# Kernel tuning notes

Measured on AMD Instinct MI355X. Metric: run time of the kernel, lower is better.

Reference implementation:

```python
import jax, jax.numpy as jnp
import numpy as np


def conv1d(x, w, b, pad):
    # x: [B, C, L], w: [O, C, K], torch nn.Conv1d semantics (cross-correlation + bias)
    y = jax.lax.conv_general_dilated(
        x, w, window_strides=(1,), padding=[(pad, pad)],
        dimension_numbers=("NCH", "OIH", "NCH"))
    return y + b[None, :, None]


def setup_inputs() -> dict:
    key = jax.random.key(0)
    ks = jax.random.split(key, 11)
    B, C, L = 32, 4, 65536
    def rn(k, shape, fan_in):
        # kaiming-ish scale so activations stay sane
        return jax.random.normal(k, shape, dtype=jnp.float32) / np.sqrt(fan_in)
    return {
        "x": jax.random.normal(ks[0], (B, C, L), dtype=jnp.float32),
        "w_motif": rn(ks[1], (40, 4, 51), 4 * 51),
        "b_motif": jnp.zeros((40,), jnp.float32),
        "w_reduce": rn(ks[2], (4, 40, 1), 40),
        "b_reduce": jnp.zeros((4,), jnp.float32),
        "w_fft": rn(ks[3], (4, 4, 401), 4 * 401),
        "b_fft": jnp.zeros((4,), jnp.float32),
        "w_expand": rn(ks[4], (40, 4, 1), 4),
        "b_expand": jnp.zeros((40,), jnp.float32),
        "w_effect": rn(ks[5], (2, 40, 601), 40 * 601),
        "b_effect": jnp.zeros((2,), jnp.float32),
    }


def reference(x, w_motif, b_motif, w_reduce, b_reduce, w_fft, b_fft,
              w_expand, b_expand, w_effect, b_effect):
    # motif layer + softplus
    y = jax.nn.softplus(conv1d(x, w_motif, b_motif, 25))          # [B,40,L]
    # synergy: factorized FFT-conv block (reduce 1x1 -> long conv -> expand 1x1)
    s = conv1d(y, w_reduce, b_reduce, 0)                          # [B,4,L]
    s = conv1d(s, w_fft, b_fft, 200)                              # [B,4,L]
    s = conv1d(s, w_expand, b_expand, 0)                          # [B,40,L]
    motifact = jax.nn.sigmoid(s) * y                              # gated
    # effect: long conv -> sigmoid
    y_pred = jax.nn.sigmoid(conv1d(motifact, w_effect, b_effect, 300))  # [B,2,L]
    return y_pred[:, :, 500:-500]
```

## Files before the change

kernel.cpp:

```cpp
#include <hip/hip_runtime.h>
#include <hip/hip_bf16.h>
#include <math.h>

#define LEN 65536
#define LOUT 64536
typedef __hip_bfloat16 bf16;
typedef __attribute__((ext_vector_type(8))) short short8;
typedef __attribute__((ext_vector_type(4))) float f32x4;

__device__ inline float b2f(bf16 h) { return __bfloat162float(h); }
__device__ inline bf16 f2b(float f) { return __float2bfloat16(f); }
__device__ inline float us2f(unsigned short u) { bf16 h = *(bf16*)&u; return __bfloat162float(h); }
__device__ inline float softplus_f(float v) {
    return fmaxf(v, 0.f) + __logf(1.f + __expf(-fabsf(v)));
}

__global__ __launch_bounds__(256) void k_x2b(const float* __restrict__ x,
                                             short* __restrict__ xb, int n8) {
    int i = blockIdx.x * 256 + threadIdx.x;
    if (i >= n8) return;
    const float* src = x + (size_t)i * 8;
    float4 f0 = *(const float4*)src;
    float4 f1 = *(const float4*)(src + 4);
    short8 v; bf16 h;
    h = f2b(f0.x); v[0] = *(short*)&h;
    h = f2b(f0.y); v[1] = *(short*)&h;
    h = f2b(f0.z); v[2] = *(short*)&h;
    h = f2b(f0.w); v[3] = *(short*)&h;
    h = f2b(f1.x); v[4] = *(short*)&h;
    h = f2b(f1.y); v[5] = *(short*)&h;
    h = f2b(f1.z); v[6] = *(short*)&h;
    h = f2b(f1.w); v[7] = *(short*)&h;
    *(short8*)(xb + (size_t)i * 8) = v;
}

__global__ __launch_bounds__(256) void k_prep_mot(const float* __restrict__ w_motif,
                                                  short* __restrict__ fragA) {
    int idx = blockIdx.x * 256 + threadIdx.x;
    if (idx >= 40 * 4 * 3 * 64 * 8) return;
    int i = idx & 7;
    int lane = (idx >> 3) & 63;
    int rest = idx >> 9;
    int qc = rest % 3; rest /= 3;
    int c = rest & 3; int o = rest >> 2;
    int dlt = lane & 15, kb = lane >> 4;
    int m = 32 * qc + 8 * kb + i;
    int k = m - 7 - dlt;
    float v = (k >= 0 && k < 51) ? w_motif[(o * 4 + c) * 51 + k] : 0.f;
    bf16 h = f2b(v);
    fragA[idx] = *(short*)&h;
}

#define MOT_BLKS 522
#define MOT_PAD  528
__global__ __launch_bounds__(256, 2) void k_motif_mfma(const short* __restrict__ xb,
        const short* __restrict__ fragA, const float* __restrict__ b_motif,
        bf16* __restrict__ y, int b0) {
    __shared__ __align__(16) short bwin[4][MOT_PAD * 8];
    const int tid = threadIdx.x;
    const int lane = tid & 63, wv = tid >> 6;
    const int wg = blockIdx.x, bl = blockIdx.y, og = blockIdx.z;
    const int bg = b0 + bl;
    const int L0 = wg * 4096;
    const int win0 = L0 - 32;
    const int ln15 = lane & 15, lkb = lane >> 4;

    short8 af[4][12];
    #pragma unroll
    for (int Mt = 0; Mt < 4; ++Mt)
        #pragma unroll
        for (int kq = 0; kq < 12; ++kq)
            af[Mt][kq] = *(const short8*)(fragA +
                (size_t)(((og * 4 + Mt) * 12 + kq) * 64 + lane) * 8);

    #pragma unroll 1
    for (int c = 0; c < 4; ++c) {
        const short* src = xb + ((size_t)bg * 4 + c) * LEN;
        for (int Lb = tid; Lb < MOT_BLKS; Lb += 256) {
            int gi = win0 + Lb * 8;
            short8 v;
            if (gi >= 0 && gi + 8 <= LEN) {
                v = *(const short8*)(src + gi);
            } else {
                #pragma unroll
                for (int j = 0; j < 8; ++j)
                    v[j] = (gi + j >= 0 && gi + j < LEN) ? src[gi + j] : (short)0;
            }
            int Pb = Lb ^ ((Lb >> 3) & 7);
            *(short8*)(&bwin[c][Pb * 8]) = v;
        }
    }
    __syncthreads();

    #pragma unroll 1
    for (int nt = 0; nt < 4; ++nt) {
        const int tt = wv * 4 + nt;
        f32x4 acc[4];
        #pragma unroll
        for (int Mt = 0; Mt < 4; ++Mt) acc[Mt] = (f32x4){0.f, 0.f, 0.f, 0.f};
        #pragma unroll
        for (int c = 0; c < 4; ++c) {
            #pragma unroll
            for (int qc = 0; qc < 3; ++qc) {
                int L = 32 * tt + 2 * ln15 + 4 * qc + lkb;
                int P = L ^ ((L >> 3) & 7);
                short8 bfr = *(const short8*)(&bwin[c][P * 8]);
                #pragma unroll
                for (int Mt = 0; Mt < 4; ++Mt)
                    acc[Mt] = __builtin_amdgcn_mfma_f32_16x16x32_bf16(
                        af[Mt][c * 3 + qc], bfr, acc[Mt], 0, 0, 0);
            }
        }
        #pragma unroll
        for (int Mt = 0; Mt < 4; ++Mt) {
            float bb = b_motif[og * 4 + Mt];
            int pos = L0 + tt * 256 + 16 * ln15 + 4 * lkb;
            ushort4 st; bf16 h;
            float v0 = softplus_f(acc[Mt][0] + bb);
            float v1 = softplus_f(acc[Mt][1] + bb);
            float v2 = softplus_f(acc[Mt][2] + bb);
            float v3 = softplus_f(acc[Mt][3] + bb);
            h = f2b(v0); st.x = *(unsigned short*)&h;
            h = f2b(v1); st.y = *(unsigned short*)&h;
            h = f2b(v2); st.z = *(unsigned short*)&h;
            h = f2b(v3); st.w = *(unsigned short*)&h;
            *(ushort4*)(&y[((size_t)bl * 40 + og * 4 + Mt) * LEN + pos]) = st;
        }
    }
}

__global__ __launch_bounds__(256) void k_reduce(const short* __restrict__ y,
        const float* __restrict__ w_reduce, const float* __restrict__ b_reduce,
        bf16* __restrict__ s1) {
    const int tid = threadIdx.x;
    const int bl = blockIdx.y;
    const int l8 = (blockIdx.x * 256 + tid) * 8;
    float s[4][8];
    #pragma unroll
    for (int c = 0; c < 4; ++c)
        #pragma unroll
        for (int e = 0; e < 8; ++e) s[c][e] = b_reduce[c];
    #pragma unroll 1
    for (int o = 0; o < 40; ++o) {
        short8 v = *(const short8*)(y + ((size_t)bl * 40 + o) * LEN + l8);
        float yv[8];
        #pragma unroll
        for (int e = 0; e < 8; ++e) yv[e] = us2f((unsigned short)v[e]);
        #pragma unroll
        for (int c = 0; c < 4; ++c) {
            float w = w_reduce[c * 40 + o];
            #pragma unroll
            for (int e = 0; e < 8; ++e) s[c][e] += w * yv[e];
        }
    }
    #pragma unroll
    for (int c = 0; c < 4; ++c) {
        short8 st; bf16 h;
        #pragma unroll
        for (int e = 0; e < 8; ++e) { h = f2b(s[c][e]); st[e] = *(short*)&h; }
        *(short8*)(&s1[((size_t)bl * 4 + c) * LEN + l8]) = st;
    }
}

__global__ __launch_bounds__(256) void k_prep_fft(const float* __restrict__ w_fft,
                                                  short* __restrict__ fragA) {
    int idx = blockIdx.x * 256 + threadIdx.x;
    if (idx >= 4 * 7 * 4 * 2 * 64 * 8) return;
    int i = idx & 7;
    int lane = (idx >> 3) & 63;
    int rest = idx >> 9;
    int ql = rest & 1; rest >>= 1;
    int Mt = rest & 3; rest >>= 2;
    int qb = rest % 7; int c = rest / 7;
    int dlt = lane & 15, kb = lane >> 4;
    int kkp = 32 * (qb * 2 + ql) + 8 * kb + i;
    int kk = kkp - dlt;
    float v = (kk >= 0 && kk < 401) ? w_fft[(Mt * 4 + c) * 401 + kk] : 0.f;
    bf16 h = f2b(v);
    fragA[idx] = *(short*)&h;
}

#define FFT_BLKS 568
__global__ __launch_bounds__(256) void k_fft(const short* __restrict__ s1,
        const short* __restrict__ fragA, const float* __restrict__ b_fft,
        bf16* __restrict__ s2) {
    __shared__ __align__(16) short bwin[4][FFT_BLKS * 8];
    const int tid = threadIdx.x;
    const int lane = tid & 63, wv = tid >> 6;
    const int wg = blockIdx.x, bl = blockIdx.y;
    const int P0 = wg * 4096;
    const int win0 = P0 - 200;
    const int ln15 = lane & 15, lkb = lane >> 4;

    f32x4 acc[4][4];
    #pragma unroll
    for (int Mt = 0; Mt < 4; ++Mt)
        #pragma unroll
        for (int nt = 0; nt < 4; ++nt)
            acc[Mt][nt] = (f32x4){0.f, 0.f, 0.f, 0.f};

    #pragma unroll 1
    for (int cl = 0; cl < 4; ++cl) {
        const short* src = s1 + ((size_t)bl * 4 + cl) * LEN;
        for (int Lb = tid; Lb < FFT_BLKS; Lb += 256) {
            int gi = win0 + Lb * 8;
            short8 v;
            if (gi >= 0 && gi + 8 <= LEN) {
                v = *(const short8*)(src + gi);
            } else {
                #pragma unroll
                for (int j = 0; j < 8; ++j)
                    v[j] = (gi + j >= 0 && gi + j < LEN) ? src[gi + j] : (short)0;
            }
            int Pb = Lb ^ ((Lb >> 3) & 7);
            *(short8*)(&bwin[cl][Pb * 8]) = v;
        }
    }
    __syncthreads();

    #pragma unroll 1
    for (int cl = 0; cl < 4; ++cl) {
        #pragma unroll 1
        for (int qb = 0; qb < 7; ++qb) {
            short8 af[4][2];
            #pragma unroll
            for (int Mt = 0; Mt < 4; ++Mt)
                #pragma unroll
                for (int ql = 0; ql < 2; ++ql)
                    af[Mt][ql] = *(const short8*)(fragA +
                        (size_t)((((cl * 7 + qb) * 4 + Mt) * 2 + ql) * 64 + lane) * 8);
            #pragma unroll
            for (int nt = 0; nt < 4; ++nt) {
                const int tt = wv * 4 + nt;
                #pragma unroll
                for (int ql = 0; ql < 2; ++ql) {
                    int qc = qb * 2 + ql;
                    int L = 2 * ln15 + lkb + 4 * qc + 32 * tt;
                    int P = L ^ ((L >> 3) & 7);
                    short8 bfr = *(const short8*)(&bwin[cl][P * 8]);
                    #pragma unroll
                    for (int Mt = 0; Mt < 4; ++Mt)
                        acc[Mt][nt] = __builtin_amdgcn_mfma_f32_16x16x32_bf16(
                            af[Mt][ql], bfr, acc[Mt][nt], 0, 0, 0);
                }
            }
        }
    }

    #pragma unroll
    for (int Mt = 0; Mt < 4; ++Mt) {
        float bb = b_fft[Mt];
        #pragma unroll
        for (int nt = 0; nt < 4; ++nt) {
            int tt = wv * 4 + nt;
            int pos = P0 + tt * 256 + 16 * ln15 + 4 * lkb;
            ushort4 st; bf16 h;
            h = f2b(acc[Mt][nt][0] + bb); st.x = *(unsigned short*)&h;
            h = f2b(acc[Mt][nt][1] + bb); st.y = *(unsigned short*)&h;
            h = f2b(acc[Mt][nt][2] + bb); st.z = *(unsigned short*)&h;
            h = f2b(acc[Mt][nt][3] + bb); st.w = *(unsigned short*)&h;
            *(ushort4*)(&s2[((size_t)bl * 4 + Mt) * LEN + pos]) = st;
        }
    }
}

__global__ __launch_bounds__(256) void k_prep(const float* __restrict__ w_eff,
                                              short* __restrict__ fragA) {
    int idx = blockIdx.x * 256 + threadIdx.x;
    if (idx >= 40 * 4 * 2 * 5 * 64 * 8) return;
    int i = idx & 7;
    int lane = (idx >> 3) & 63;
    int rest = idx >> 9;
    int ql = rest % 5; rest /= 5;
    int Mt = rest & 1; rest >>= 1;
    int qb = rest & 3; int c = rest >> 2;
    int q = qb * 5 + ql;
    int dlt = lane & 15, kb = lane >> 4;
    int kp = 32 * q + 8 * kb + i;
    int kk = kp - dlt;
    float v = (kk >= 0 && kk < 601) ? w_eff[(Mt * 40 + c) * 601 + kk] : 0.f;
    bf16 h = __float2bfloat16(v);
    fragA[idx] = *(short*)&h;
}

#define EFF_NBLK 336
#define EFF_SH (EFF_NBLK * 8)
__device__ __forceinline__ void eff_prefetch(const short* __restrict__ mact,
        size_t chanBase, int cc, int tid, int win0, short8 (&yreg)[2][4]) {
    #pragma unroll
    for (int it = 0; it < 2; ++it) {
        int Lb = tid + it * 256;
        if (Lb < EFF_NBLK) {
            int gi = win0 + Lb * 8;
            bool full = (gi + 8 <= LEN);
            #pragma unroll
            for (int ch = 0; ch < 4; ++ch) {
                const short* src = mact + (chanBase + cc * 4 + ch) * (size_t)LEN;
                short8 v = {0, 0, 0, 0, 0, 0, 0, 0};
                if (full) {
                    v = *(const short8*)(src + gi);
                } else {
                    #pragma unroll
                    for (int j = 0; j < 8; ++j)
                        v[j] = (gi + j < LEN) ? src[gi + j] : (short)0;
                }
                yreg[it][ch] = v;
            }
        }
    }
}

__global__ __launch_bounds__(256, 3) void k_effect(const short* __restrict__ mact,
        const short* __restrict__ s2,
        const short* __restrict__ fragA,
        const float* __restrict__ w_expand, const float* __restrict__ b_expand,
        float* __restrict__ part) {
    __shared__ __align__(16) char smem[2 * EFF_SH * 4 * 2 + 160 * 4 + 40 * 4];
    short (*bwin)[EFF_SH]  = (short(*)[EFF_SH])smem;
    short (*s2win)[EFF_SH] = (short(*)[EFF_SH])(smem + EFF_SH * 4 * 2);
    float* wexp = (float*)(smem + 2 * EFF_SH * 4 * 2);
    float* bexp = wexp + 160;
    float* red  = (float*)smem;

    const int tid = threadIdx.x;
    const int lane = tid & 63, wv = tid >> 6;
    const int wgl = blockIdx.x, bl = blockIdx.y, half = blockIdx.z;
    const int coff = half * 20;
    const int L0 = wgl * 2048;
    const int win0 = L0 + 200;
    const int ln15 = lane & 15, lkb = lane >> 4;
    const size_t chanBase = (size_t)bl * 40 + coff;

    if (tid < 160) wexp[tid] = w_expand[tid];
    if (tid < 40) bexp[tid] = b_expand[tid];
    #pragma unroll 1
    for (int c = 0; c < 4; ++c) {
        const short* sp = s2 + ((size_t)bl * 4 + c) * LEN;
        for (int Lb = tid; Lb < EFF_NBLK; Lb += 256) {
            int gi = win0 + Lb * 8;
            short8 v = {0, 0, 0, 0, 0, 0, 0, 0};
            if (gi + 8 <= LEN) {
                v = *(const short8*)(sp + gi);
            } else {
                #pragma unroll
                for (int j = 0; j < 8; ++j)
                    v[j] = (gi + j < LEN) ? sp[gi + j] : (short)0;
            }
            *(short8*)(&s2win[c][Lb * 8]) = v;
        }
    }

    f32x4 acc[2][8];
    #pragma unroll
    for (int Mt = 0; Mt < 2; ++Mt)
        #pragma unroll
        for (int tt = 0; tt < 8; ++tt)
            acc[Mt][tt] = (f32x4){0.f, 0.f, 0.f, 0.f};

    short8 yreg[2][4];
    eff_prefetch(mact, chanBase, 0, tid, win0, yreg);

    #pragma unroll 1
    for (int cc = 0; cc < 5; ++cc) {
        __syncthreads();
        #pragma unroll
        for (int it = 0; it < 2; ++it) {
            int Lb = tid + it * 256;
            if (Lb < EFF_NBLK) {
                float s2v[4][8];
                #pragma unroll
                for (int c = 0; c < 4; ++c) {
                    short8 sv = *(const short8*)(&s2win[c][Lb * 8]);
                    #pragma unroll
                    for (int j = 0; j < 8; ++j) s2v[c][j] = us2f((unsigned short)sv[j]);
                }
                int P = Lb ^ ((Lb >> 3) & 7);
                #pragma unroll
                for (int ch = 0; ch < 4; ++ch) {
                    int o = coff + cc * 4 + ch;
                    float w0 = wexp[o * 4 + 0], w1 = wexp[o * 4 + 1];
                    float w2 = wexp[o * 4 + 2], w3 = wexp[o * 4 + 3];
                    float be = bexp[o];
                    short8 w;
                    #pragma unroll
                    for (int j = 0; j < 8; ++j) {
                        float sg = be + w0 * s2v[0][j] + w1 * s2v[1][j]
                                      + w2 * s2v[2][j] + w3 * s2v[3][j];
                        float g = __builtin_amdgcn_rcpf(1.f + __expf(-sg));
                        float yv = us2f((unsigned short)yreg[it][ch][j]) * g;
                        bf16 h = f2b(yv);
                        w[j] = *(short*)&h;
                    }
                    *(short8*)(&bwin[ch][P * 8]) = w;
                }
            }
        }
        __syncthreads();
        if (cc < 4) eff_prefetch(mact, chanBase, cc + 1, tid, win0, yreg);
        const int cg = coff + cc * 4 + wv;
        #pragma unroll 1
        for (int qb = 0; qb < 4; ++qb) {
            short8 af[2][5];
            #pragma unroll
            for (int Mt = 0; Mt < 2; ++Mt)
                #pragma unroll
                for (int ql = 0; ql < 5; ++ql)
                    af[Mt][ql] = *(const short8*)(fragA +
                        (size_t)(((((cg * 4 + qb) * 2 + Mt) * 5 + ql) * 64 + lane) * 8));
            #pragma unroll
            for (int tt = 0; tt < 8; ++tt) {
                #pragma unroll
                for (int ql = 0; ql < 5; ++ql) {
                    int q = qb * 5 + ql;
                    int L = 32 * tt + 2 * ln15 + 4 * q + lkb;
                    int P = L ^ ((L >> 3) & 7);
                    short8 bfr = *(const short8*)(&bwin[wv][P * 8]);
                    acc[0][tt] = __builtin_amdgcn_mfma_f32_16x16x32_bf16(
                        af[0][ql], bfr, acc[0][tt], 0, 0, 0);
                    acc[1][tt] = __builtin_amdgcn_mfma_f32_16x16x32_bf16(
                        af[1][ql], bfr, acc[1][tt], 0, 0, 0);
                }
            }
        }
    }

    __syncthreads();
    if (wv == 1 || wv == 3) {
        float* p = red + (wv >> 1) * 4096;
        #pragma unroll
        for (int Mt = 0; Mt < 2; ++Mt)
            #pragma unroll
            for (int tt = 0; tt < 8; ++tt)
                *(f32x4*)(p + (Mt * 8 + tt) * 256 + lane * 4) = acc[Mt][tt];
    }
    __syncthreads();
    if (wv == 0 || wv == 2) {
        float* p = red + (wv >> 1) * 4096;
        #pragma unroll
        for (int Mt = 0; Mt < 2; ++Mt)
            #pragma unroll
            for (int tt = 0; tt < 8; ++tt)
                acc[Mt][tt] += *(const f32x4*)(p + (Mt * 8 + tt) * 256 + lane * 4);
    }
    __syncthreads();
    if (wv == 2) {
        #pragma unroll
        for (int Mt = 0; Mt < 2; ++Mt)
            #pragma unroll
            for (int tt = 0; tt < 8; ++tt)
                *(f32x4*)(red + (Mt * 8 + tt) * 256 + lane * 4) = acc[Mt][tt];
    }
    __syncthreads();
    if (wv == 0) {
        #pragma unroll
        for (int Mt = 0; Mt < 2; ++Mt) {
            #pragma unroll
            for (int tt = 0; tt < 8; ++tt) {
                f32x4 a = acc[Mt][tt];
                a += *(const f32x4*)(red + (Mt * 8 + tt) * 256 + lane * 4);
                int pos = L0 + tt * 256 + 16 * ln15 + 4 * lkb;
                float4 st; st.x = a[0]; st.y = a[1]; st.z = a[2]; st.w = a[3];
                *(float4*)(&part[(((size_t)bl * 2 + half) * 2 + Mt) * LEN + pos]) = st;
            }
        }
    }
}

__global__ __launch_bounds__(256) void k_comb(const float* __restrict__ part,
        const float* __restrict__ b_eff, float* __restrict__ out, int b0) {
    const int tid = threadIdx.x;
    const int bl = blockIdx.y, bg = b0 + bl;
    int l4 = (blockIdx.x * 256 + tid) * 4;
    if (l4 >= LOUT) return;
    #pragma unroll
    for (int Mt = 0; Mt < 2; ++Mt) {
        float bb = b_eff[Mt];
        float4 p0 = *(const float4*)(&part[(((size_t)bl * 2 + 0) * 2 + Mt) * LEN + l4]);
        float4 p1 = *(const float4*)(&part[(((size_t)bl * 2 + 1) * 2 + Mt) * LEN + l4]);
        float4 st;
        st.x = __builtin_amdgcn_rcpf(1.f + __expf(-(p0.x + p1.x + bb)));
        st.y = __builtin_amdgcn_rcpf(1.f + __expf(-(p0.y + p1.y + bb)));
        st.z = __builtin_amdgcn_rcpf(1.f + __expf(-(p0.z + p1.z + bb)));
        st.w = __builtin_amdgcn_rcpf(1.f + __expf(-(p0.w + p1.w + bb)));
        *(float4*)(&out[((size_t)bg * 2 + Mt) * LOUT + l4]) = st;
    }
}

extern "C" void kernel_launch(void* const* d_in, const int* in_sizes, int n_in,
                              void* d_out, int out_size, void* d_ws, size_t ws_size,
                              hipStream_t stream) {
    const float* x        = (const float*)d_in[0];
    const float* w_motif  = (const float*)d_in[1];
    const float* b_motif  = (const float*)d_in[2];
    const float* w_reduce = (const float*)d_in[3];
    const float* b_reduce = (const float*)d_in[4];
    const float* w_fft    = (const float*)d_in[5];
    const float* b_fft    = (const float*)d_in[6];
    const float* w_expand = (const float*)d_in[7];
    const float* b_expand = (const float*)d_in[8];
    const float* w_eff    = (const float*)d_in[9];
    const float* b_eff    = (const float*)d_in[10];
    float* out = (float*)d_out;

    const size_t FRAGA_EFF = (size_t)40 * 4 * 2 * 5 * 64 * 8 * 2;
    const size_t FRAGA_FFT = (size_t)4 * 7 * 4 * 2 * 64 * 8 * 2;
    const size_t FRAGA_MOT = (size_t)40 * 4 * 3 * 64 * 8 * 2;
    const size_t XB_B      = (size_t)32 * 4 * LEN * 2;
    const size_t HEAD = FRAGA_EFF + FRAGA_FFT + FRAGA_MOT + XB_B;

    short* fragA_eff = (short*)d_ws;
    short* fragA_fft = (short*)((char*)d_ws + FRAGA_EFF);
    short* fragA_mot = (short*)((char*)d_ws + FRAGA_EFF + FRAGA_FFT);
    short* xb        = (short*)((char*)d_ws + FRAGA_EFF + FRAGA_FFT + FRAGA_MOT);
    char*  rest      = (char*)d_ws + HEAD;

    const size_t PB_Y = (size_t)40 * LEN * 2;
    const size_t PB_S = (size_t)4 * LEN * 2;
    const size_t PERB = PB_Y + 2 * PB_S + (size_t)2 * 2 * LEN * 4;
    size_t avail = (ws_size > HEAD) ? (ws_size - HEAD) : 0;
    int nb = (int)(avail / PERB);
    if (nb > 32) nb = 32;
    if (nb < 1) nb = 1;

    bf16*  y    = (bf16*)rest;
    bf16*  s1   = (bf16*)(rest + PB_Y * (size_t)nb);
    bf16*  s2   = (bf16*)(rest + (PB_Y + PB_S) * (size_t)nb);
    float* part = (float*)(rest + (PB_Y + 2 * PB_S) * (size_t)nb);

    hipLaunchKernelGGL(k_prep,     dim3(3200), dim3(256), 0, stream, w_eff, fragA_eff);
    hipLaunchKernelGGL(k_prep_fft, dim3(448),  dim3(256), 0, stream, w_fft, fragA_fft);
    hipLaunchKernelGGL(k_prep_mot, dim3(960),  dim3(256), 0, stream, w_motif, fragA_mot);
    hipLaunchKernelGGL(k_x2b,      dim3(4096), dim3(256), 0, stream, x, xb,
                       (int)(32 * 4 * LEN / 8));

    for (int b0 = 0; b0 < 32; b0 += nb) {
        int nbb = (32 - b0 < nb) ? (32 - b0) : nb;
        hipLaunchKernelGGL(k_motif_mfma, dim3(16, nbb, 10), dim3(256), 0, stream,
                           xb, fragA_mot, b_motif, y, b0);
        hipLaunchKernelGGL(k_reduce, dim3(32, nbb), dim3(256), 0, stream,
                           (const short*)y, w_reduce, b_reduce, s1);
        hipLaunchKernelGGL(k_fft, dim3(16, nbb), dim3(256), 0, stream,
                           (const short*)s1, fragA_fft, b_fft, s2);
        hipLaunchKernelGGL(k_effect, dim3(32, nbb, 2), dim3(256), 0, stream,
                           (const short*)y, (const short*)s2, fragA_eff,
                           w_expand, b_expand, part);
        hipLaunchKernelGGL(k_comb, dim3(64, nbb), dim3(256), 0, stream,
                           part, b_eff, out, b0);
    }
}
```

Measured before the change: 435.5 us.

## Fuse 1x1 reduce conv into motif MFMA kernel epilogue

The motif kernel now loops over all 10 output-channel groups inside one block instead of splitting them across the grid. It accumulates the 40->4 reduce projection in registers from the softplus outputs and writes s1 directly, which removes the separate k_reduce kernel and its re-read of y. In exchange the grid shrinks tenfold (16 x nbb blocks), which may hurt occupancy and parallelism. The motif A-fragments are now reloaded per channel, and register pressure rises with 16 accumulators plus 64 s1 partial sums. The s1 sums also use fp32 softplus values rather than bf16-rounded y, a small numerical difference.

```diff
diff --git a/kernel.cpp b/kernel.cpp
--- a/kernel.cpp
+++ b/kernel.cpp
@@ -55,23 +55,16 @@
 #define MOT_PAD  528
 __global__ __launch_bounds__(256, 2) void k_motif_mfma(const short* __restrict__ xb,
         const short* __restrict__ fragA, const float* __restrict__ b_motif,
-        bf16* __restrict__ y, int b0) {
+        const float* __restrict__ w_reduce, const float* __restrict__ b_reduce,
+        bf16* __restrict__ y, bf16* __restrict__ s1, int b0) {
     __shared__ __align__(16) short bwin[4][MOT_PAD * 8];
     const int tid = threadIdx.x;
     const int lane = tid & 63, wv = tid >> 6;
-    const int wg = blockIdx.x, bl = blockIdx.y, og = blockIdx.z;
+    const int wg = blockIdx.x, bl = blockIdx.y;
     const int bg = b0 + bl;
     const int L0 = wg * 4096;
     const int win0 = L0 - 32;
     const int ln15 = lane & 15, lkb = lane >> 4;
-
-    short8 af[4][12];
-    #pragma unroll
-    for (int Mt = 0; Mt < 4; ++Mt)
-        #pragma unroll
-        for (int kq = 0; kq < 12; ++kq)
-            af[Mt][kq] = *(const short8*)(fragA +
-                (size_t)(((og * 4 + Mt) * 12 + kq) * 64 + lane) * 8);
 
     #pragma unroll 1
     for (int c = 0; c < 4; ++c) {
@@ -92,73 +85,95 @@
     }
     __syncthreads();
 
+    float s1a[4][4][4];
+    #pragma unroll
+    for (int nt = 0; nt < 4; ++nt)
+        #pragma unroll
+        for (int c = 0; c < 4; ++c) {
+            float bc = b_reduce[c];
+            #pragma unroll
+            for (int j = 0; j < 4; ++j) s1a[nt][c][j] = bc;
+        }
+
     #pragma unroll 1
+    for (int og = 0; og < 10; ++og) {
+        f32x4 acc[4][4];
+        #pragma unroll
+        for (int Mt = 0; Mt < 4; ++Mt)
+            #pragma unroll
+            for (int nt = 0; nt < 4; ++nt)
+                acc[Mt][nt] = (f32x4){0.f, 0.f, 0.f, 0.f};
+
+        #pragma unroll 1
+        for (int c = 0; c < 4; ++c) {
+            short8 afc[4][3];
+            #pragma unroll
+            for (int Mt = 0; Mt < 4; ++Mt)
+                #pragma unroll
+                for (int qc = 0; qc < 3; ++qc)
+                    afc[Mt][qc] = *(const short8*)(fragA +
+                        (size_t)(((og * 4 + Mt) * 12 + c * 3 + qc) * 64 + lane) * 8);
+            #pragma unroll
+            for (int nt = 0; nt < 4; ++nt) {
+                const int tt = wv * 4 + nt;
+                #pragma unroll
+                for (int qc = 0; qc < 3; ++qc) {
+                    int L = 32 * tt + 2 * ln15 + 4 * qc + lkb;
+                    int P = L ^ ((L >> 3) & 7);
+                    short8 bfr = *(const short8*)(&bwin[c][P * 8]);
+                    #pragma unroll
+                    for (int Mt = 0; Mt < 4; ++Mt)
+                        acc[Mt][nt] = __builtin_amdgcn_mfma_f32_16x16x32_bf16(
+                            afc[Mt][qc], bfr, acc[Mt][nt], 0, 0, 0);
+                }
+            }
+        }
+
+        #pragma unroll
+        for (int Mt = 0; Mt < 4; ++Mt) {
+            const int o = og * 4 + Mt;
+            const float bb = b_motif[o];
+            const float wr0 = w_reduce[0 * 40 + o], wr1 = w_reduce[1 * 40 + o];
+            const float wr2 = w_reduce[2 * 40 + o], wr3 = w_reduce[3 * 40 + o];
+            #pragma unroll
+            for (int nt = 0; nt < 4; ++nt) {
+                int tt = wv * 4 + nt;
+                int pos = L0 + tt * 256 + 16 * ln15 + 4 * lkb;
+                float v0 = softplus_f(acc[Mt][nt][0] + bb);
+                float v1 = softplus_f(acc[Mt][nt][1] + bb);
+                float v2 = softplus_f(acc[Mt][nt][2] + bb);
+                float v3 = softplus_f(acc[Mt][nt][3] + bb);
+                ushort4 st; bf16 h;
+                h = f2b(v0); st.x = *(unsigned short*)&h;
+                h = f2b(v1); st.y = *(unsigned short*)&h;
+                h = f2b(v2); st.z = *(unsigned short*)&h;
+                h = f2b(v3); st.w = *(unsigned short*)&h;
+                *(ushort4*)(&y[((size_t)bl * 40 + o) * LEN + pos]) = st;
+                s1a[nt][0][0] += wr0 * v0; s1a[nt][0][1] += wr0 * v1;
+                s1a[nt][0][2] += wr0 * v2; s1a[nt][0][3] += wr0 * v3;
+                s1a[nt][1][0] += wr1 * v0; s1a[nt][1][1] += wr1 * v1;
+                s1a[nt][1][2] += wr1 * v2; s1a[nt][1][3] += wr1 * v3;
+                s1a[nt][2][0] += wr2 * v0; s1a[nt][2][1] += wr2 * v1;
+                s1a[nt][2][2] += wr2 * v2; s1a[nt][2][3] += wr2 * v3;
+                s1a[nt][3][0] += wr3 * v0; s1a[nt][3][1] += wr3 * v1;
+                s1a[nt][3][2] += wr3 * v2; s1a[nt][3][3] += wr3 * v3;
+            }
+        }
+    }
+
+    #pragma unroll
     for (int nt = 0; nt < 4; ++nt) {
-        const int tt = wv * 4 + nt;
-        f32x4 acc[4];
-        #pragma unroll
-        for (int Mt = 0; Mt < 4; ++Mt) acc[Mt] = (f32x4){0.f, 0.f, 0.f, 0.f};
+        int tt = wv * 4 + nt;
+        int pos = L0 + tt * 256 + 16 * ln15 + 4 * lkb;
         #pragma unroll
         for (int c = 0; c < 4; ++c) {
-            #pragma unroll
-            for (int qc = 0; qc < 3; ++qc) {
-                int L = 32 * tt + 2 * ln15 + 4 * qc + lkb;
-                int P = L ^ ((L >> 3) & 7);
-                short8 bfr = *(const short8*)(&bwin[c][P * 8]);
-                #pragma unroll
-                for (int Mt = 0; Mt < 4; ++Mt)
-                    acc[Mt] = __builtin_amdgcn_mfma_f32_16x16x32_bf16(
-                        af[Mt][c * 3 + qc], bfr, acc[Mt], 0, 0, 0);
-            }
-        }
-        #pragma unroll
-        for (int Mt = 0; Mt < 4; ++Mt) {
-            float bb = b_motif[og * 4 + Mt];
-            int pos = L0 + tt * 256 + 16 * ln15 + 4 * lkb;
             ushort4 st; bf16 h;
-            float v0 = softplus_f(acc[Mt][0] + bb);
-            float v1 = softplus_f(acc[Mt][1] + bb);
-            float v2 = softplus_f(acc[Mt][2] + bb);
-            float v3 = softplus_f(acc[Mt][3] + bb);
-            h = f2b(v0); st.x = *(unsigned short*)&h;
-            h = f2b(v1); st.y = *(unsigned short*)&h;
-            h = f2b(v2); st.z = *(unsigned short*)&h;
-            h = f2b(v3); st.w = *(unsigned short*)&h;
-            *(ushort4*)(&y[((size_t)bl * 40 + og * 4 + Mt) * LEN + pos]) = st;
-        }
-    }
-}
-
-__global__ __launch_bounds__(256) void k_reduce(const short* __restrict__ y,
-        const float* __restrict__ w_reduce, const float* __restrict__ b_reduce,
-        bf16* __restrict__ s1) {
-    const int tid = threadIdx.x;
-    const int bl = blockIdx.y;
-    const int l8 = (blockIdx.x * 256 + tid) * 8;
-    float s[4][8];
-    #pragma unroll
-    for (int c = 0; c < 4; ++c)
-        #pragma unroll
-        for (int e = 0; e < 8; ++e) s[c][e] = b_reduce[c];
-    #pragma unroll 1
-    for (int o = 0; o < 40; ++o) {
-        short8 v = *(const short8*)(y + ((size_t)bl * 40 + o) * LEN + l8);
-        float yv[8];
-        #pragma unroll
-        for (int e = 0; e < 8; ++e) yv[e] = us2f((unsigned short)v[e]);
-        #pragma unroll
-        for (int c = 0; c < 4; ++c) {
-            float w = w_reduce[c * 40 + o];
-            #pragma unroll
-            for (int e = 0; e < 8; ++e) s[c][e] += w * yv[e];
-        }
-    }
-    #pragma unroll
-    for (int c = 0; c < 4; ++c) {
-        short8 st; bf16 h;
-        #pragma unroll
-        for (int e = 0; e < 8; ++e) { h = f2b(s[c][e]); st[e] = *(short*)&h; }
-        *(short8*)(&s1[((size_t)bl * 4 + c) * LEN + l8]) = st;
+            h = f2b(s1a[nt][c][0]); st.x = *(unsigned short*)&h;
+            h = f2b(s1a[nt][c][1]); st.y = *(unsigned short*)&h;
+            h = f2b(s1a[nt][c][2]); st.z = *(unsigned short*)&h;
+            h = f2b(s1a[nt][c][3]); st.w = *(unsigned short*)&h;
+            *(ushort4*)(&s1[((size_t)bl * 4 + c) * LEN + pos]) = st;
+        }
     }
 }
 
@@ -535,10 +550,8 @@
 
     for (int b0 = 0; b0 < 32; b0 += nb) {
         int nbb = (32 - b0 < nb) ? (32 - b0) : nb;
-        hipLaunchKernelGGL(k_motif_mfma, dim3(16, nbb, 10), dim3(256), 0, stream,
-                           xb, fragA_mot, b_motif, y, b0);
-        hipLaunchKernelGGL(k_reduce, dim3(32, nbb), dim3(256), 0, stream,
-                           (const short*)y, w_reduce, b_reduce, s1);
+        hipLaunchKernelGGL(k_motif_mfma, dim3(16, nbb), dim3(256), 0, stream,
+                           xb, fragA_mot, b_motif, w_reduce, b_reduce, y, s1, b0);
         hipLaunchKernelGGL(k_fft, dim3(16, nbb), dim3(256), 0, stream,
                            (const short*)s1, fragA_fft, b_fft, s2);
         hipLaunchKernelGGL(k_effect, dim3(32, nbb, 2), dim3(256), 0, stream,
```

Measured after the change: 393.2 us (median of 2 runs). 9.7% less time.
